# Optimization experiments

Measured on AMD Instinct MI355X. Metric: run time of the kernel, lower is better.

The kernel has to match this reference:

```python
import jax, jax.numpy as jnp
import numpy as np

B, S, D, DA, H = 4, 2048, 1024, 1024, 16
DH = DA // H  # 64, per-head dim (tensor_split on last dim == contiguous head chunks)


def setup_inputs() -> dict:
    key = jax.random.key(0)
    ks = jax.random.split(key, 8)
    init = 0.02
    return {
        "q": jax.random.normal(ks[0], (B, S, D), jnp.float32),
        "k": jax.random.normal(ks[1], (B, S, D), jnp.float32),
        "v": jax.random.normal(ks[2], (B, S, D), jnp.float32),
        "mask": jnp.ones((B, 1, S), jnp.int32),
        "w_q": jax.random.normal(ks[3], (DA, D), jnp.float32) * init,
        "b_q": jnp.zeros((DA,), jnp.float32),
        "w_k": jax.random.normal(ks[4], (DA, D), jnp.float32) * init,
        "b_k": jnp.zeros((DA,), jnp.float32),
        "w_v": jax.random.normal(ks[5], (DA, D), jnp.float32) * init,
        "b_v": jnp.zeros((DA,), jnp.float32),
        "w_o": jax.random.normal(ks[6], (D, DA), jnp.float32) * init,
        "b_o": jnp.zeros((D,), jnp.float32),
    }


def reference(q, k, v, mask, w_q, b_q, w_k, b_k, w_v, b_v, w_o, b_o):
    # projections (nn.Linear: x @ W.T + b)
    xq = q @ w_q.T + b_q            # [B,S,DA]
    xk = k @ w_k.T + b_k
    xv = v @ w_v.T + b_v
    # tensor_split into h contiguous chunks == reshape to [B,S,H,DH]
    xq = xq.reshape(B, S, H, DH)
    xk = xk.reshape(B, S, H, DH)
    xv = xv.reshape(B, S, H, DH)
    scores = jnp.einsum('bqhd,bkhd->bhqk', xq, xk) / jnp.sqrt(jnp.asarray(DH, xq.dtype))
    # mask [B,1,S] broadcasts over heads and query rows -> [B,1,1,S]
    scores = jnp.where(mask[:, None] == 0, -jnp.inf, scores)
    probs = jax.nn.softmax(scores, axis=-1)  # dropout p=0.0 -> identity
    out = jnp.einsum('bhqk,bkhd->bqhd', probs, xv).reshape(B, S, DA)
    return out @ w_o.T + b_o        # [B,S,D]
```

## Files before the change

kernel.cpp:

```cpp
#include <hip/hip_runtime.h>
#include <hip/hip_bf16.h>
#include <cstdint>
#include <cstddef>

typedef __bf16 bf16;
typedef __attribute__((ext_vector_type(8))) __bf16 bf16x8;
typedef __attribute__((ext_vector_type(4))) __bf16 bf16x4;
typedef __attribute__((ext_vector_type(4))) float f32x4;
typedef __attribute__((ext_vector_type(4))) int i32x4;

#define MFMA_BF16(a, b, c) __builtin_amdgcn_mfma_f32_16x16x32_bf16((a), (b), (c), 0, 0, 0)

constexpr int CB = 4;
constexpr int CS = 2048;
constexpr int CD = 1024;
constexpr int CDA = 1024;
constexpr int CH = 16;
constexpr int CM = CB * CS;
constexpr int NT = CS / 64;

__global__ __launch_bounds__(256) void cvt_w4(
    const float* __restrict__ s0, const float* __restrict__ s1,
    const float* __restrict__ s2, const float* __restrict__ s3,
    bf16* __restrict__ dst)
{
    int bid = blockIdx.x;
    int m = bid >> 9;
    size_t li = ((size_t)(bid & 511) * 256 + threadIdx.x) * 8;
    const float* s = (m == 0) ? s0 : (m == 1) ? s1 : (m == 2) ? s2 : s3;
    f32x4 a = *(const f32x4*)(s + li);
    f32x4 c = *(const f32x4*)(s + li + 4);
    bf16x8 o;
#pragma unroll
    for (int j = 0; j < 4; ++j) { o[j] = (bf16)a[j]; o[4 + j] = (bf16)c[j]; }
    *(bf16x8*)(dst + (size_t)m * (CD * CDA) + li) = o;
}

template <int AMODE, int OMODE>
__global__ __launch_bounds__(256) void gemm_nt_bias(
    const void* __restrict__ Ap, const bf16* __restrict__ W,
    const float* __restrict__ bias, void* __restrict__ Cp,
    int M, int N, int K)
{
    __shared__ __align__(16) char smem[32768];
    char* As = smem;
    char* Bs = smem + 16384;

    const int t = threadIdx.x;
    const int lane = t & 63;
    const int wid = t >> 6;
    const int wr = wid >> 1, wc = wid & 1;
    const int l15 = lane & 15, lg = lane >> 4;
    const int m0 = blockIdx.x * 128;
    const int n0 = blockIdx.y * 128;

    f32x4 acc[4][4] = {};

    for (int k0 = 0; k0 < K; k0 += 64) {
        if (AMODE == 0) {
            const float* A = (const float*)Ap;
#pragma unroll
            for (int i = 0; i < 8; ++i) {
                int chunk = t + i * 256;
                int row = chunk >> 4, c4 = (chunk & 15) * 4;
                f32x4 v = *(const f32x4*)(A + (size_t)(m0 + row) * K + k0 + c4);
                bf16x4 o;
#pragma unroll
                for (int jj = 0; jj < 4; ++jj) o[jj] = (bf16)v[jj];
                *(bf16x4*)(As + row * 128 + (((c4 >> 3) ^ (row & 7)) << 4) +
                           ((c4 & 4) << 1)) = o;
            }
        } else {
            const bf16* A = (const bf16*)Ap;
#pragma unroll
            for (int i = 0; i < 4; ++i) {
                int chunk = t + i * 256;
                int row = chunk >> 3, slot = chunk & 7;
                const bf16* src = A + (size_t)(m0 + row) * K + k0 + ((slot ^ (row & 7)) << 3);
                __builtin_amdgcn_global_load_lds(
                    (const __attribute__((address_space(1))) void*)src,
                    (__attribute__((address_space(3))) void*)(As + ((i * 256 + wid * 64) << 4)),
                    16, 0, 0);
            }
        }
#pragma unroll
        for (int i = 0; i < 4; ++i) {
            int chunk = t + i * 256;
            int row = chunk >> 3, slot = chunk & 7;
            const bf16* src = W + (size_t)(n0 + row) * K + k0 + ((slot ^ (row & 7)) << 3);
            __builtin_amdgcn_global_load_lds(
                (const __attribute__((address_space(1))) void*)src,
                (__attribute__((address_space(3))) void*)(Bs + ((i * 256 + wid * 64) << 4)),
                16, 0, 0);
        }
        __syncthreads();

#pragma unroll
        for (int kk = 0; kk < 64; kk += 32) {
            bf16x8 af[4], bfv[4];
#pragma unroll
            for (int mi = 0; mi < 4; ++mi) {
                int row = wr * 64 + mi * 16 + l15;
                af[mi] = *(const bf16x8*)(As + row * 128 +
                                          ((((kk >> 3) + lg) ^ (row & 7)) << 4));
            }
#pragma unroll
            for (int ni = 0; ni < 4; ++ni) {
                int row = wc * 64 + ni * 16 + l15;
                bfv[ni] = *(const bf16x8*)(Bs + row * 128 +
                                           ((((kk >> 3) + lg) ^ (row & 7)) << 4));
            }
#pragma unroll
            for (int mi = 0; mi < 4; ++mi)
#pragma unroll
                for (int ni = 0; ni < 4; ++ni)
                    acc[mi][ni] = MFMA_BF16(af[mi], bfv[ni], acc[mi][ni]);
        }
        __syncthreads();
    }

    if (OMODE == 2) {
        bf16* C = (bf16*)Cp;
        const int mblock = m0 + wr * 64;
#pragma unroll
        for (int ni = 0; ni < 4; ++ni) {
            int n = n0 + wc * 64 + ni * 16 + l15;
            float bv = bias[n];
#pragma unroll
            for (int mi = 0; mi < 4; ++mi) {
                int s = mi * 16 + lg * 4;
                int cps = (s & 32) | ((s & 12) << 1) | ((s & 16) >> 2);
                bf16x4 o;
#pragma unroll
                for (int r = 0; r < 4; ++r) o[r] = (bf16)(acc[mi][ni][r] + bv);
                *(bf16x4*)(C + (size_t)n * CM + mblock + cps) = o;
            }
        }
    } else {
#pragma unroll
        for (int ni = 0; ni < 4; ++ni) {
            int col = n0 + wc * 64 + ni * 16 + l15;
            float bv = bias[col];
#pragma unroll
            for (int mi = 0; mi < 4; ++mi) {
#pragma unroll
                for (int r = 0; r < 4; ++r) {
                    int row = m0 + wr * 64 + mi * 16 + lg * 4 + r;
                    float val = acc[mi][ni][r] + bv;
                    if (OMODE == 1)
                        ((float*)Cp)[(size_t)row * N + col] = val;
                    else
                        ((bf16*)Cp)[(size_t)row * N + col] = (bf16)val;
                }
            }
        }
    }
}

__global__ __launch_bounds__(512, 4) void attn_kernel(
    const bf16* __restrict__ xq, const bf16* __restrict__ xk,
    const bf16* __restrict__ xvT, const int* __restrict__ mask,
    bf16* __restrict__ out)
{
    __shared__ __align__(16) char smem[32768];

    const int t = threadIdx.x;
    const int lane = t & 63;
    const int wid = t >> 6;
    const int l15 = lane & 15, lg = lane >> 4;
    const int g = blockIdx.x;
    const int j = g >> 3;
    const int bh = (g & 7) * 8 + (j & 7);
    const int qt = j >> 3;
    const int b = bh >> 4, h = bh & 15;
    const int q0 = qt * 256;
    constexpr float SCL = 0.125f * 1.44269504088896340736f;
    constexpr float M2 = 12.0f * SCL;

    const int sub = lane >> 3;
    const int sb  = (lane & 7) ^ sub;
    const bf16* kbase = xk + (size_t)(b * CS + wid * 8 + sub) * CDA + h * 64 + sb * 8;
    const bf16* vbase = xvT + (size_t)(h * 64 + wid * 8 + sub) * CM + b * CS + sb * 8;

#define STAGE(bufi, ktt)                                                           \
    {                                                                              \
        char* Kd = smem + (bufi) * 16384 + wid * 1024;                             \
        char* Vd = smem + (bufi) * 16384 + 8192 + wid * 1024;                      \
        __builtin_amdgcn_global_load_lds(                                          \
            (const __attribute__((address_space(1))) void*)(kbase + (size_t)(ktt) * 64 * CDA), \
            (__attribute__((address_space(3))) void*)Kd, 16, 0, 0);                \
        __builtin_amdgcn_global_load_lds(                                          \
            (const __attribute__((address_space(1))) void*)(vbase + (ktt) * 64),   \
            (__attribute__((address_space(3))) void*)Vd, 16, 0, 0);                \
    }

    bf16x8 aq[2][2];
#pragma unroll
    for (int mi = 0; mi < 2; ++mi)
#pragma unroll
        for (int kh = 0; kh < 2; ++kh) {
            bf16x8 v = *(const bf16x8*)(xq +
                (size_t)(b * CS + q0 + wid * 32 + mi * 16 + l15) * CDA + h * 64 + kh * 32 + lg * 8);
#pragma unroll
            for (int jj = 0; jj < 8; ++jj) v[jj] = (bf16)((float)v[jj] * SCL);
            aq[mi][kh] = v;
        }

    bf16x8 onescol;
    {
        bf16 fv = (l15 == 0) ? (bf16)1.0f : (bf16)0.0f;
#pragma unroll
        for (int jj = 0; jj < 8; ++jj) onescol[jj] = fv;
    }

    f32x4 accO[2][5] = {};

    STAGE(0, 0);
    __syncthreads();

    for (int kt = 0; kt < NT; ++kt) {
        const int cur = kt & 1;
        char* Ksb = smem + cur * 16384;
        char* Vtb = Ksb + 8192;

        f32x4 mb[4];
#pragma unroll
        for (int ni = 0; ni < 4; ++ni) {
            i32x4 mk = *(const i32x4*)(mask + b * CS + kt * 64 + ni * 16 + lg * 4);
#pragma unroll
            for (int r = 0; r < 4; ++r)
                mb[ni][r] = (mk[r] == 0) ? -1.0e30f : -M2;
        }

        if (kt + 1 < NT) STAGE(cur ^ 1, kt + 1);

        f32x4 sT[4][2];
#pragma unroll
        for (int ni = 0; ni < 4; ++ni) { sT[ni][0] = mb[ni]; sT[ni][1] = mb[ni]; }
#pragma unroll
        for (int kh = 0; kh < 2; ++kh) {
            bf16x8 bk[4];
#pragma unroll
            for (int ni = 0; ni < 4; ++ni) {
                int key = ni * 16 + l15;
                bk[ni] = *(const bf16x8*)(Ksb + key * 128 +
                                          ((kh * 64 + lg * 16) ^ ((key & 7) << 4)));
            }
#pragma unroll
            for (int ni = 0; ni < 4; ++ni)
#pragma unroll
                for (int mi = 0; mi < 2; ++mi)
                    sT[ni][mi] = MFMA_BF16(bk[ni], aq[mi][kh], sT[ni][mi]);
        }

#pragma unroll
        for (int ni = 0; ni < 4; ++ni)
#pragma unroll
            for (int mi = 0; mi < 2; ++mi)
#pragma unroll
                for (int r = 0; r < 4; ++r)
                    sT[ni][mi][r] = exp2f(sT[ni][mi][r]);

        bf16x8 ap[2][2];
#pragma unroll
        for (int kks = 0; kks < 2; ++kks)
#pragma unroll
            for (int mi = 0; mi < 2; ++mi)
#pragma unroll
                for (int r = 0; r < 4; ++r) {
                    ap[kks][mi][r]     = (bf16)sT[2 * kks][mi][r];
                    ap[kks][mi][4 + r] = (bf16)sT[2 * kks + 1][mi][r];
                }

#pragma unroll
        for (int kks = 0; kks < 2; ++kks) {
            bf16x8 bv[4];
#pragma unroll
            for (int di = 0; di < 4; ++di) {
                int d = di * 16 + l15;
                bv[di] = *(const bf16x8*)(Vtb + d * 128 +
                                          ((kks * 64 + lg * 16) ^ ((d & 7) << 4)));
            }
#pragma unroll
            for (int mi = 0; mi < 2; ++mi) {
#pragma unroll
                for (int di = 0; di < 4; ++di)
                    accO[mi][di] = MFMA_BF16(ap[kks][mi], bv[di], accO[mi][di]);
                accO[mi][4] = MFMA_BF16(ap[kks][mi], onescol, accO[mi][4]);
            }
        }

        __syncthreads();
    }
#undef STAGE

    char* Ob = smem + wid * 2048;
#pragma unroll
    for (int mi = 0; mi < 2; ++mi) {
#pragma unroll
        for (int r = 0; r < 4; ++r) {
            float lsum = __shfl(accO[mi][4][r], lane & 48);
            float inv = 1.0f / lsum;
            int qr = lg * 4 + r;
#pragma unroll
            for (int di = 0; di < 4; ++di)
                *(bf16*)(Ob + qr * 128 + (((di * 16 + l15) * 2) ^ ((qr & 7) << 4))) =
                    (bf16)(accO[mi][di][r] * inv);
        }
        __builtin_amdgcn_sched_barrier(0);
#pragma unroll
        for (int i = 0; i < 2; ++i) {
            int rr = i * 8 + (lane >> 3);
            int ch = lane & 7;
            bf16x8 o = *(const bf16x8*)(Ob + rr * 128 + ((ch * 16) ^ ((rr & 7) << 4)));
            *(bf16x8*)(out + (size_t)(b * CS + q0 + wid * 32 + mi * 16 + rr) * CDA +
                       h * 64 + ch * 8) = o;
        }
        __builtin_amdgcn_sched_barrier(0);
    }
}

extern "C" void kernel_launch(void* const* d_in, const int* in_sizes, int n_in,
                              void* d_out, int out_size, void* d_ws, size_t ws_size,
                              hipStream_t stream)
{
    const float* q   = (const float*)d_in[0];
    const float* k   = (const float*)d_in[1];
    const float* v   = (const float*)d_in[2];
    const int*   msk = (const int*)d_in[3];
    const float* w_q = (const float*)d_in[4];
    const float* b_q = (const float*)d_in[5];
    const float* w_k = (const float*)d_in[6];
    const float* b_k = (const float*)d_in[7];
    const float* w_v = (const float*)d_in[8];
    const float* b_v = (const float*)d_in[9];
    const float* w_o = (const float*)d_in[10];
    const float* b_o = (const float*)d_in[11];

    bf16* xq  = (bf16*)d_ws;
    bf16* xk  = xq + (size_t)CM * CDA;
    bf16* xvT = xk + (size_t)CM * CDA;
    bf16* at  = xvT + (size_t)CM * CDA;
    bf16* wb  = at + (size_t)CM * CDA;

    cvt_w4<<<dim3(2048), 256, 0, stream>>>(w_q, w_k, w_v, w_o, wb);

    const size_t WSZ = (size_t)CD * CDA;
    dim3 gp(CM / 128, CDA / 128);
    gemm_nt_bias<0, 0><<<gp, 256, 0, stream>>>((const void*)q, wb,           b_q, (void*)xq,  CM, CDA, CD);
    gemm_nt_bias<0, 0><<<gp, 256, 0, stream>>>((const void*)k, wb + WSZ,     b_k, (void*)xk,  CM, CDA, CD);
    gemm_nt_bias<0, 2><<<gp, 256, 0, stream>>>((const void*)v, wb + 2 * WSZ, b_v, (void*)xvT, CM, CDA, CD);

    attn_kernel<<<dim3(512), 512, 0, stream>>>(xq, xk, xvT, msk, at);

    gemm_nt_bias<1, 1><<<dim3(CM / 128, CD / 128), 256, 0, stream>>>(
        (const void*)at, wb + 3 * WSZ, b_o, d_out, CM, CD, CDA);
}
```

Before: 223.8 us.

## Swap GEMM grid order, cache mask bias in LDS, precompute LDS offsets, add setprio

The projection and output GEMMs now index the grid with N-tiles on blockIdx.x, so consecutive blocks share the same activation rows and reuse them through L2. In the attention kernel the mask is converted once per block into an LDS bias table rather than read from global memory on every key tile. Swizzled LDS offsets for K and V are computed once before the loop, the next-tile prefetch is issued earlier, and the MFMA clusters are wrapped in s_setprio to favour matrix issue. These changes cost 8 KB more LDS per block and more registers for the offset arrays, which may reduce occupancy.

```diff
diff --git a/kernel.cpp b/kernel.cpp
--- a/kernel.cpp
+++ b/kernel.cpp
@@ -51,8 +51,8 @@
     const int wid = t >> 6;
     const int wr = wid >> 1, wc = wid & 1;
     const int l15 = lane & 15, lg = lane >> 4;
-    const int m0 = blockIdx.x * 128;
-    const int n0 = blockIdx.y * 128;
+    const int m0 = blockIdx.y * 128;
+    const int n0 = blockIdx.x * 128;
 
     f32x4 acc[4][4] = {};
 
@@ -162,7 +162,8 @@
     const bf16* __restrict__ xvT, const int* __restrict__ mask,
     bf16* __restrict__ out)
 {
-    __shared__ __align__(16) char smem[32768];
+    __shared__ __align__(16) char smem[40960];
+    float* Mb = (float*)(smem + 32768);
 
     const int t = threadIdx.x;
     const int lane = t & 63;
@@ -194,6 +195,14 @@
             (__attribute__((address_space(3))) void*)Vd, 16, 0, 0);                \
     }
 
+    {
+        i32x4 mk = *(const i32x4*)(mask + b * CS + t * 4);
+        f32x4 o;
+#pragma unroll
+        for (int r = 0; r < 4; ++r) o[r] = (mk[r] == 0) ? -1.0e30f : -M2;
+        *(f32x4*)(Mb + t * 4) = o;
+    }
+
     bf16x8 aq[2][2];
 #pragma unroll
     for (int mi = 0; mi < 2; ++mi)
@@ -213,6 +222,22 @@
         for (int jj = 0; jj < 8; ++jj) onescol[jj] = fv;
     }
 
+    int koff[2][4], voff[2][4];
+#pragma unroll
+    for (int kh = 0; kh < 2; ++kh)
+#pragma unroll
+        for (int ni = 0; ni < 4; ++ni) {
+            int key = ni * 16 + l15;
+            koff[kh][ni] = key * 128 + ((kh * 64 + lg * 16) ^ ((key & 7) << 4));
+        }
+#pragma unroll
+    for (int kks = 0; kks < 2; ++kks)
+#pragma unroll
+        for (int di = 0; di < 4; ++di) {
+            int d = di * 16 + l15;
+            voff[kks][di] = 8192 + d * 128 + ((kks * 64 + lg * 16) ^ ((d & 7) << 4));
+        }
+
     f32x4 accO[2][5] = {};
 
     STAGE(0, 0);
@@ -220,19 +245,14 @@
 
     for (int kt = 0; kt < NT; ++kt) {
         const int cur = kt & 1;
-        char* Ksb = smem + cur * 16384;
-        char* Vtb = Ksb + 8192;
+        char* buf = smem + cur * 16384;
+
+        if (kt + 1 < NT) STAGE(cur ^ 1, kt + 1);
 
         f32x4 mb[4];
 #pragma unroll
-        for (int ni = 0; ni < 4; ++ni) {
-            i32x4 mk = *(const i32x4*)(mask + b * CS + kt * 64 + ni * 16 + lg * 4);
-#pragma unroll
-            for (int r = 0; r < 4; ++r)
-                mb[ni][r] = (mk[r] == 0) ? -1.0e30f : -M2;
-        }
-
-        if (kt + 1 < NT) STAGE(cur ^ 1, kt + 1);
+        for (int ni = 0; ni < 4; ++ni)
+            mb[ni] = *(const f32x4*)(Mb + kt * 64 + ni * 16 + lg * 4);
 
         f32x4 sT[4][2];
 #pragma unroll
@@ -241,16 +261,15 @@
         for (int kh = 0; kh < 2; ++kh) {
             bf16x8 bk[4];
 #pragma unroll
-            for (int ni = 0; ni < 4; ++ni) {
-                int key = ni * 16 + l15;
-                bk[ni] = *(const bf16x8*)(Ksb + key * 128 +
-                                          ((kh * 64 + lg * 16) ^ ((key & 7) << 4)));
-            }
+            for (int ni = 0; ni < 4; ++ni)
+                bk[ni] = *(const bf16x8*)(buf + koff[kh][ni]);
+            __builtin_amdgcn_s_setprio(1);
 #pragma unroll
             for (int ni = 0; ni < 4; ++ni)
 #pragma unroll
                 for (int mi = 0; mi < 2; ++mi)
                     sT[ni][mi] = MFMA_BF16(bk[ni], aq[mi][kh], sT[ni][mi]);
+            __builtin_amdgcn_s_setprio(0);
         }
 
 #pragma unroll
@@ -276,11 +295,9 @@
         for (int kks = 0; kks < 2; ++kks) {
             bf16x8 bv[4];
 #pragma unroll
-            for (int di = 0; di < 4; ++di) {
-                int d = di * 16 + l15;
-                bv[di] = *(const bf16x8*)(Vtb + d * 128 +
-                                          ((kks * 64 + lg * 16) ^ ((d & 7) << 4)));
-            }
+            for (int di = 0; di < 4; ++di)
+                bv[di] = *(const bf16x8*)(buf + voff[kks][di]);
+            __builtin_amdgcn_s_setprio(1);
 #pragma unroll
             for (int mi = 0; mi < 2; ++mi) {
 #pragma unroll
@@ -288,6 +305,7 @@
                     accO[mi][di] = MFMA_BF16(ap[kks][mi], bv[di], accO[mi][di]);
                 accO[mi][4] = MFMA_BF16(ap[kks][mi], onescol, accO[mi][4]);
             }
+            __builtin_amdgcn_s_setprio(0);
         }
 
         __syncthreads();
@@ -346,13 +364,13 @@
     cvt_w4<<<dim3(2048), 256, 0, stream>>>(w_q, w_k, w_v, w_o, wb);
 
     const size_t WSZ = (size_t)CD * CDA;
-    dim3 gp(CM / 128, CDA / 128);
+    dim3 gp(CDA / 128, CM / 128);
     gemm_nt_bias<0, 0><<<gp, 256, 0, stream>>>((const void*)q, wb,           b_q, (void*)xq,  CM, CDA, CD);
     gemm_nt_bias<0, 0><<<gp, 256, 0, stream>>>((const void*)k, wb + WSZ,     b_k, (void*)xk,  CM, CDA, CD);
     gemm_nt_bias<0, 2><<<gp, 256, 0, stream>>>((const void*)v, wb + 2 * WSZ, b_v, (void*)xvT, CM, CDA, CD);
 
     attn_kernel<<<dim3(512), 512, 0, stream>>>(xq, xk, xvT, msk, at);
 
-    gemm_nt_bias<1, 1><<<dim3(CM / 128, CD / 128), 256, 0, stream>>>(
+    gemm_nt_bias<1, 1><<<dim3(CD / 128, CM / 128), 256, 0, stream>>>(
         (const void*)at, wb + 3 * WSZ, b_o, d_out, CM, CD, CDA);
 }
```

After: 256.3 us. +14.5%, slower.
